# Optimization experiments

Hardware: AMD Instinct MI355X
Metric: run time of the kernel (lower is better)

## Reference

```python
import jax, jax.numpy as jnp
import numpy as np

B, S, D, DS, NSLOT = 2, 1024, 1024, 320, 512
H, CH = 4, 5
DFF = 4 * D
MAXIT = 2


def _ln(x, g, b, eps=1e-5):
    m = x.mean(-1, keepdims=True)
    v = ((x - m) ** 2).mean(-1, keepdims=True)
    return (x - m) * jax.lax.rsqrt(v + eps) * g + b


def _mha(x, Wq, Wk, Wv, Wo, bq, bk, bv, bo, nh):
    b_, s_, d_ = x.shape
    hd = d_ // nh
    q = (x @ Wq + bq).reshape(b_, s_, nh, hd)
    k = (x @ Wk + bk).reshape(b_, s_, nh, hd)
    v = (x @ Wv + bv).reshape(b_, s_, nh, hd)
    a = jax.nn.softmax(jnp.einsum('bqhd,bkhd->bhqk', q, k) * (hd ** -0.5), axis=-1)
    o = jnp.einsum('bhqk,bkhd->bqhd', a, v).reshape(b_, s_, d_)
    return o @ Wo + bo


def setup_inputs():
    key = jax.random.key(0)
    ks = iter(jax.random.split(key, 64))
    n = lambda shape: jax.random.normal(next(ks), shape, jnp.float32) * 0.02
    z = lambda shape: jnp.zeros(shape, jnp.float32)
    o = lambda shape: jnp.ones(shape, jnp.float32)
    return dict(
        x=jax.random.normal(next(ks), (B, S, D), jnp.float32),
        cache=jax.random.normal(next(ks), (B, NSLOT, DS), jnp.float32),
        iter_emb=n((16, D)),
        rq_w=n((D, D)), rg_w=n((D, 1)), rg_b=z((1,)), ck_w=n((DS, D)), cv_w=n((DS, D)),
        aq_w=n((D, D)), ak_w=n((D, D)), av_w=n((D, D)), ao_w=n((D, D)),
        aq_b=z((D,)), ak_b=z((D,)), av_b=z((D,)), ao_b=z((D,)),
        f1_w=n((D, DFF)), f1_b=z((DFF,)), f2_w=n((DFF, D)), f2_b=z((D,)),
        n1_g=o((D,)), n1_b=z((D,)), n2_g=o((D,)), n2_b=z((D,)),
        sq_w=n((DS, DS)), tk_w=n((D, DS)), tv_w=n((D, DS)), wg_w=n((D, 1)), wg_b=z((1,)),
        cq_w=n((DS, DS)), ck2_w=n((DS, DS)), cv2_w=n((DS, DS)), co_w=n((DS, DS)),
        cq_b=z((DS,)), ck2_b=z((DS,)), cv2_b=z((DS,)), co_b=z((DS,)),
        cn_g=o((DS,)), cn_b=z((DS,)),
        max_iterations=MAXIT,
    )


def reference(x, cache, iter_emb, rq_w, rg_w, rg_b, ck_w, cv_w,
              aq_w, ak_w, av_w, ao_w, aq_b, ak_b, av_b, ao_b,
              f1_w, f1_b, f2_w, f2_b, n1_g, n1_b, n2_g, n2_b,
              sq_w, tk_w, tv_w, wg_w, wg_b,
              cq_w, ck2_w, cv2_w, co_w, cq_b, ck2_b, cv2_b, co_b, cn_g, cn_b,
              max_iterations):
    def mem_read(h, cc):
        # gather from cache: gated cross-attention readout
        q = h @ rq_w                                   # [B,S,D]
        k = cc @ ck_w                                  # [B,N,D]
        v = cc @ cv_w                                  # [B,N,D]
        a = jax.nn.softmax(jnp.einsum('bsd,bnd->bsn', q, k) * (D ** -0.5), axis=-1)
        readout = jnp.einsum('bsn,bnd->bsd', a, v)
        gate = jax.nn.sigmoid(h @ rg_w + rg_b)          # [B,S,1] soft read gate
        return h + gate * readout

    def compute_block(h):
        # faithful to ComputeBlock (non-linear-attention branch): norm1 used twice
        hn = _ln(h, n1_g, n1_b)
        attn = _mha(hn, aq_w, ak_w, av_w, ao_w, aq_b, ak_b, av_b, ao_b, H)
        h = _ln(h + attn, n1_g, n1_b)
        ffn = jax.nn.gelu(h @ f1_w + f1_b) @ f2_w + f2_b
        return _ln(h + ffn, n2_g, n2_b)

    def mem_write(h, cc):
        # importance-scored scatter: slots attend over tokens, gated by importance
        sq = cc @ sq_w                                  # [B,N,DS]
        tk = h @ tk_w                                   # [B,S,DS]
        tv = h @ tv_w                                   # [B,S,DS]
        gate = jax.nn.sigmoid(h @ wg_w + wg_b)          # [B,S,1] soft write gate
        a = jax.nn.softmax(jnp.einsum('bnd,bsd->bns', sq, tk) * (DS ** -0.5), axis=-1)
        upd = jnp.einsum('bns,bsd->bnd', a, gate * tv)
        return cc + upd

    def cache_self_attn(cc):
        attn = _mha(cc, cq_w, ck2_w, cv2_w, co_w, cq_b, ck2_b, cv2_b, co_b, CH)
        return _ln(cc + attn, cn_g, cn_b)

    h = x
    cc = cache
    layer_input = x
    h_prev = None
    for it in range(max_iterations):
        h = h + iter_emb[it][None, None, :]
        if it > 0:
            h = h + layer_input + h_prev
        h_enh = mem_read(h, cc)
        h_comp = compute_block(h_enh)
        cc = mem_write(h_comp, cc)
        cc = cache_self_attn(cc)
        h = h_comp
        h_prev = jax.lax.stop_gradient(h_comp)  # torch: h_prev = h_computed.detach()
    return h
```

## Files before the change

### kernel.cpp

```cpp
#include <hip/hip_runtime.h>
#include <cstdint>

constexpr int B_ = 2, S_ = 1024, D_ = 1024, DS_ = 320, NSLOT_ = 512;
constexpr int H_ = 4, CH_ = 5, DFF_ = 4096;
constexpr int HD_ = D_ / H_;
constexpr int CHD_ = DS_ / CH_;
constexpr int BS_ = B_ * S_;
constexpr int BNS_ = B_ * NSLOT_;

typedef unsigned short u16;
typedef __attribute__((ext_vector_type(8))) short bf16x8;
typedef __attribute__((ext_vector_type(4))) float f32x4;
typedef __attribute__((ext_vector_type(4))) u16 u16x4;
typedef long long ll;

__device__ __forceinline__ u16 f2bf(float f) {
  unsigned u = __float_as_uint(f);
  return (u16)((u + 0x7FFFu + ((u >> 16) & 1u)) >> 16);
}
__device__ __forceinline__ float bf2f(u16 h) { return __uint_as_float((unsigned)h << 16); }

__device__ __forceinline__ void gload16(const void* g, void* l) {
  __builtin_amdgcn_global_load_lds((const __attribute__((address_space(1))) void*)g,
                                   (__attribute__((address_space(3))) void*)l, 16, 0, 0);
}

template<int BN>
__global__ __launch_bounds__(512, 4)
void k_gemm(const u16* __restrict__ A, int lda, ll sA, ll sA2,
            const u16* __restrict__ Bp, int ldb, ll sB, ll sB2,
            float* __restrict__ outF, u16* __restrict__ outB,
            int ldc, ll sC, ll sC2,
            u16* __restrict__ outBT, int ldt, ll sT, ll sT2,
            int K, int zdiv, const float* __restrict__ bias,
            const float* __restrict__ rowscale, int rscfrom,
            int splitcol, int act)
{
  constexpr int BM = 128;
  constexpr int MI = (BN == 128) ? 2 : 1;
  constexpr int NI = 4;
  constexpr int WROWS = MI * 16;
  constexpr int ABYT = BM * 128;
  constexpr int BBYT = BN * 128;
  constexpr int BUF = ABYT + BBYT;
  const int z = blockIdx.z, zb = z / zdiv, zr = z - zb * zdiv;
  A  += (ll)zb * sA + (ll)zr * sA2;
  Bp += (ll)zb * sB + (ll)zr * sB2;
  const ll cof = (ll)zb * sC + (ll)zr * sC2;
  const ll tof = (ll)zb * sT + (ll)zr * sT2;
  const int bm = blockIdx.y * BM, bn = blockIdx.x * BN;
  __shared__ __align__(16) char lds[2 * BUF];
  const int tid = threadIdx.x;
  const int lane = tid & 63, wid = tid >> 6;
  const int wm = (BN == 128) ? (wid >> 1) : wid;
  const int wn = (BN == 128) ? (wid & 1) : 0;
  const int rowb = wm * WROWS, colb = wn * 64;

  f32x4 acc[MI][NI];
  const f32x4 fz = {0.f, 0.f, 0.f, 0.f};
  #pragma unroll
  for (int i = 0; i < MI; ++i)
    #pragma unroll
    for (int j = 0; j < NI; ++j) acc[i][j] = fz;

  const int trow = tid >> 3;
  const int tg   = ((tid & 7) ^ (trow & 7)) * 8;
  const u16* gA  = A + (ll)(bm + trow) * lda + tg;
  const u16* gA2 = gA + (ll)64 * lda;
  const u16* gB  = Bp + (ll)(bn + trow) * ldb + tg;
  const u16* gB2 = gB + (ll)64 * ldb;

  const int r = lane & 15, q = lane >> 4;
  const int c7 = r & 7;
  const int gs0 = ((q) ^ c7) << 4;
  const int gs1 = ((4 + q) ^ c7) << 4;
  int aoff[MI], boff[NI];
  #pragma unroll
  for (int i = 0; i < MI; ++i) aoff[i] = (rowb + i * 16 + r) * 128;
  #pragma unroll
  for (int j = 0; j < NI; ++j) boff[j] = (colb + j * 16 + r) * 128;

  auto stage = [&](int buf, int it) {
    char* la = lds + buf * BUF + wid * 1024;
    char* lb = la + ABYT;
    const int ko = it << 6;
    gload16(gA + ko, la);
    gload16(gA2 + ko, la + 8192);
    gload16(gB + ko, lb);
    if constexpr (BN == 128) gload16(gB2 + ko, lb + 8192);
  };

  const int nsteps = K >> 6;
  stage(0, 0);
  int bufp = 0;
  for (int it = 0; it < nsteps; ++it) {
    asm volatile("s_waitcnt vmcnt(0)" ::: "memory");
    __builtin_amdgcn_s_barrier();
    __builtin_amdgcn_sched_barrier(0);
    if (it + 1 < nsteps) stage(bufp ^ 1, it + 1);
    const char* pa = lds + bufp * BUF;
    const char* pb = pa + ABYT;
    #pragma unroll
    for (int s = 0; s < 2; ++s) {
      const int gso = s ? gs1 : gs0;
      bf16x8 af[MI], bv[NI];
      #pragma unroll
      for (int i = 0; i < MI; ++i) af[i] = *(const bf16x8*)(pa + aoff[i] + gso);
      #pragma unroll
      for (int j = 0; j < NI; ++j) bv[j] = *(const bf16x8*)(pb + boff[j] + gso);
      #pragma unroll
      for (int i = 0; i < MI; ++i)
        #pragma unroll
        for (int j = 0; j < NI; ++j)
          acc[i][j] = __builtin_amdgcn_mfma_f32_16x16x32_bf16(af[i], bv[j], acc[i][j], 0, 0, 0);
    }
    asm volatile("s_waitcnt lgkmcnt(0)" ::: "memory");
    __builtin_amdgcn_sched_barrier(0);
    bufp ^= 1;
  }

  const int fr = lane & 15, fq = lane >> 4;
  #pragma unroll
  for (int i = 0; i < MI; ++i) {
    const int r0 = bm + rowb + i * 16 + fq * 4;
    #pragma unroll
    for (int j = 0; j < NI; ++j) {
      const int cn = bn + colb + j * 16 + fr;
      const float bvv = bias ? bias[cn] : 0.f;
      const bool doRs = rowscale && (cn >= rscfrom);
      float vv[4];
      #pragma unroll
      for (int t = 0; t < 4; ++t) {
        float v = acc[i][j][t] + bvv;
        if (doRs) v *= rowscale[r0 + t];
        if (act) v = 0.5f * v * (1.f + tanhf(0.7978845608028654f * (v + 0.044715f * v * v * v)));
        vv[t] = v;
      }
      if (cn < splitcol) {
        if (outF) {
          #pragma unroll
          for (int t = 0; t < 4; ++t) outF[cof + (ll)(r0 + t) * ldc + cn] = vv[t];
        }
        if (outB) {
          #pragma unroll
          for (int t = 0; t < 4; ++t) outB[cof + (ll)(r0 + t) * ldc + cn] = f2bf(vv[t]);
        }
      } else {
        u16x4 pk = {f2bf(vv[0]), f2bf(vv[1]), f2bf(vv[2]), f2bf(vv[3])};
        *(u16x4*)(outBT + tof + (ll)(cn - splitcol) * ldt + r0) = pk;
      }
    }
  }
}

struct PrepTable {
  const float* src[16];
  u16* dst[16];
  int R[16];
  int C[16];
  int off[17];
};

__global__ __launch_bounds__(256)
void k_prep_all(PrepTable T)
{
  __shared__ float t[32][33];
  const int b = blockIdx.x;
  int w = 0;
  #pragma unroll
  for (int i = 1; i < 16; ++i) if (b >= T.off[i]) w = i;
  const int lb = b - T.off[w];
  const int tilesC = T.C[w] >> 5;
  const int by = (lb / tilesC) << 5;
  const int bx = (lb - (lb / tilesC) * tilesC) << 5;
  const float* in = T.src[w];
  u16* out = T.dst[w];
  const int R = T.R[w], C = T.C[w];
  const int tx = threadIdx.x & 31, ty = threadIdx.x >> 5;
  #pragma unroll
  for (int i = 0; i < 32; i += 8)
    t[ty + i][tx] = in[(ll)(by + ty + i) * C + bx + tx];
  __syncthreads();
  #pragma unroll
  for (int i = 0; i < 32; i += 8)
    out[(ll)(bx + ty + i) * R + by + tx] = f2bf(t[tx][ty + i]);
}

__global__ __launch_bounds__(256)
void k_cvt(const float* __restrict__ in, u16* __restrict__ out, int n)
{
  int i = blockIdx.x * 256 + threadIdx.x;
  if (i < n) out[i] = f2bf(in[i]);
}

__global__ __launch_bounds__(256)
void k_cat3f(float* __restrict__ dst, const float* __restrict__ a, int na,
             const float* __restrict__ b, int nb, const float* __restrict__ c, int nc)
{
  int i = blockIdx.x * 256 + threadIdx.x;
  if (i < na) dst[i] = a[i];
  else if (i < na + nb) dst[i] = b[i - na];
  else if (i < na + nb + nc) dst[i] = c[i - na - nb];
}

__global__ __launch_bounds__(256)
void k_softmax_b16(u16* __restrict__ x, int cols, float scale)
{
  u16* p = x + (ll)blockIdx.x * cols;
  const int tid = threadIdx.x;
  __shared__ float red[256];
  float v[4];
  float m = -1e30f;
  #pragma unroll
  for (int i = 0; i < 4; ++i) {
    const int c = tid + (i << 8);
    v[i] = (c < cols) ? bf2f(p[c]) * scale : -1e30f;
    m = fmaxf(m, v[i]);
  }
  red[tid] = m; __syncthreads();
  for (int s = 128; s > 0; s >>= 1) { if (tid < s) red[tid] = fmaxf(red[tid], red[tid + s]); __syncthreads(); }
  m = red[0]; __syncthreads();
  float sum = 0.f;
  #pragma unroll
  for (int i = 0; i < 4; ++i) { v[i] = expf(v[i] - m); sum += v[i]; }
  red[tid] = sum; __syncthreads();
  for (int s = 128; s > 0; s >>= 1) { if (tid < s) red[tid] += red[tid + s]; __syncthreads(); }
  const float inv = 1.f / red[0];
  #pragma unroll
  for (int i = 0; i < 4; ++i) {
    const int c = tid + (i << 8);
    if (c < cols) p[c] = f2bf(v[i] * inv);
  }
}

__global__ __launch_bounds__(256)
void k_layernorm(const float* __restrict__ x, const float* __restrict__ res,
                 const float* __restrict__ res2, const float* __restrict__ rbias,
                 const float* __restrict__ g, const float* __restrict__ b,
                 float* __restrict__ outF, u16* __restrict__ outB, int cols)
{
  const ll ro = (ll)blockIdx.x * cols;
  const float* px = x + ro;
  const float* pr = res ? res + ro : nullptr;
  const float* p2 = res2 ? res2 + ro : nullptr;
  __shared__ float red[256];
  const int tid = threadIdx.x;
  auto val = [&](int c) {
    float v = px[c];
    if (pr) v += pr[c];
    if (p2) v += p2[c];
    if (rbias) v += rbias[c];
    return v;
  };
  float s = 0.f;
  for (int c = tid; c < cols; c += 256) s += val(c);
  red[tid] = s; __syncthreads();
  for (int t = 128; t > 0; t >>= 1) { if (tid < t) red[tid] += red[tid + t]; __syncthreads(); }
  const float mean = red[0] / cols; __syncthreads();
  float s2 = 0.f;
  for (int c = tid; c < cols; c += 256) { float v = val(c) - mean; s2 += v * v; }
  red[tid] = s2; __syncthreads();
  for (int t = 128; t > 0; t >>= 1) { if (tid < t) red[tid] += red[tid + t]; __syncthreads(); }
  const float inv = rsqrtf(red[0] / cols + 1e-5f);
  for (int c = tid; c < cols; c += 256) {
    float v = (val(c) - mean) * inv * g[c] + b[c];
    if (outF) outF[ro + c] = v;
    if (outB) outB[ro + c] = f2bf(v);
  }
}

__global__ __launch_bounds__(256)
void k_gate_add(float* __restrict__ out, const float* __restrict__ h,
                const float* __restrict__ r, const float* __restrict__ w,
                const float* __restrict__ b0, int cols)
{
  const ll ro = (ll)blockIdx.x * cols;
  const float* ph = h + ro;
  const float* pr = r + ro;
  __shared__ float red[256];
  const int tid = threadIdx.x;
  float s = 0.f;
  for (int c = tid; c < cols; c += 256) s += ph[c] * w[c];
  red[tid] = s; __syncthreads();
  for (int t = 128; t > 0; t >>= 1) { if (tid < t) red[tid] += red[tid + t]; __syncthreads(); }
  const float g = 1.0f / (1.0f + expf(-(red[0] + b0[0])));
  for (int c = tid; c < cols; c += 256) out[ro + c] = ph[c] + g * pr[c];
}

__global__ __launch_bounds__(256)
void k_gate(const float* __restrict__ x, const float* __restrict__ w,
            const float* __restrict__ b0, float* __restrict__ out, int cols)
{
  const int lane = threadIdx.x & 63;
  const int wv = threadIdx.x >> 6;
  const ll row = (ll)blockIdx.x * 4 + wv;
  const float* p = x + row * cols;
  float s = 0.f;
  for (int c = lane; c < cols; c += 64) s += p[c] * w[c];
  #pragma unroll
  for (int off = 32; off > 0; off >>= 1) s += __shfl_down(s, off);
  if (lane == 0) out[row] = 1.0f / (1.0f + expf(-(s + b0[0])));
}

__global__ __launch_bounds__(256)
void k_combine2(float* __restrict__ oF, u16* __restrict__ oB,
                const float* __restrict__ a, float sa, const float* __restrict__ b,
                const float* __restrict__ emb, int n, int Dm1)
{
  int i = blockIdx.x * 256 + threadIdx.x;
  if (i >= n) return;
  float v = sa * a[i];
  if (b) v += b[i];
  v += emb[i & Dm1];
  oF[i] = v; oB[i] = f2bf(v);
}

__global__ __launch_bounds__(256)
void k_add2(float* __restrict__ oF, u16* __restrict__ oB,
            const float* __restrict__ a, const float* __restrict__ b, int n)
{
  int i = blockIdx.x * 256 + threadIdx.x;
  if (i >= n) return;
  float v = a[i] + b[i];
  oF[i] = v; oB[i] = f2bf(v);
}

extern "C" void kernel_launch(void* const* d_in, const int* in_sizes, int n_in,
                              void* d_out, int out_size, void* d_ws, size_t ws_size,
                              hipStream_t stream)
{
  (void)in_sizes; (void)n_in; (void)out_size;
  const float* x        = (const float*)d_in[0];
  const float* cache0   = (const float*)d_in[1];
  const float* iter_emb = (const float*)d_in[2];
  const float* rq_w     = (const float*)d_in[3];
  const float* rg_w     = (const float*)d_in[4];
  const float* rg_b     = (const float*)d_in[5];
  const float* ck_w     = (const float*)d_in[6];
  const float* cv_w     = (const float*)d_in[7];
  const float* aq_w     = (const float*)d_in[8];
  const float* ak_w     = (const float*)d_in[9];
  const float* av_w     = (const float*)d_in[10];
  const float* ao_w     = (const float*)d_in[11];
  const float* aq_b     = (const float*)d_in[12];
  const float* ak_b     = (const float*)d_in[13];
  const float* av_b     = (const float*)d_in[14];
  const float* ao_b     = (const float*)d_in[15];
  const float* f1_w     = (const float*)d_in[16];
  const float* f1_b     = (const float*)d_in[17];
  const float* f2_w     = (const float*)d_in[18];
  const float* f2_b     = (const float*)d_in[19];
  const float* n1_g     = (const float*)d_in[20];
  const float* n1_b     = (const float*)d_in[21];
  const float* n2_g     = (const float*)d_in[22];
  const float* n2_b     = (const float*)d_in[23];
  const float* sq_w     = (const float*)d_in[24];
  const float* tk_w     = (const float*)d_in[25];
  const float* tv_w     = (const float*)d_in[26];
  const float* wg_w     = (const float*)d_in[27];
  const float* wg_b     = (const float*)d_in[28];
  const float* cq_w     = (const float*)d_in[29];
  const float* ck2_w    = (const float*)d_in[30];
  const float* cv2_w    = (const float*)d_in[31];
  const float* co_w     = (const float*)d_in[32];
  const float* cq_b     = (const float*)d_in[33];
  const float* ck2_b    = (const float*)d_in[34];
  const float* cv2_b    = (const float*)d_in[35];
  const float* co_b     = (const float*)d_in[36];
  const float* cn_g     = (const float*)d_in[37];
  const float* cn_b     = (const float*)d_in[38];

  float* out = (float*)d_out;

  size_t off = 0;
  char* base = (char*)d_ws;
  auto allocF = [&](size_t n) { float* p = (float*)(base + off); off += n * 4; off = (off + 255) & ~(size_t)255; return p; };
  auto allocH = [&](size_t n) { u16* p = (u16*)(base + off); off += n * 2; off = (off + 255) & ~(size_t)255; return p; };

  float* hbuf  = allocF((size_t)BS_ * D_);
  float* henh  = allocF((size_t)BS_ * D_);
  float* hcomp = allocF((size_t)BS_ * D_);
  float* h2b   = allocF((size_t)BS_ * D_);
  float* tA    = allocF((size_t)2 * BS_ * D_);
  float* gate  = allocF((size_t)BS_);
  float* ccnf  = allocF((size_t)BNS_ * DS_);
  float* updf  = allocF((size_t)BNS_ * DS_);
  float* coo   = allocF((size_t)BNS_ * DS_);
  float* ccwf  = allocF((size_t)BNS_ * DS_);
  float* qkvb  = allocF(3 * D_);
  float* cqkvb = allocF(3 * DS_);
  u16* rqT  = allocH((size_t)D_ * D_);
  u16* ckT  = allocH((size_t)D_ * DS_);
  u16* cvT  = allocH((size_t)D_ * DS_);
  u16* aqT  = allocH((size_t)D_ * D_);
  u16* akT  = allocH((size_t)D_ * D_);
  u16* avT  = allocH((size_t)D_ * D_);
  u16* aoT  = allocH((size_t)D_ * D_);
  u16* f1T  = allocH((size_t)DFF_ * D_);
  u16* f2T  = allocH((size_t)D_ * DFF_);
  u16* sqT  = allocH((size_t)DS_ * DS_);
  u16* tkT  = allocH((size_t)DS_ * D_);
  u16* tvTw = allocH((size_t)DS_ * D_);
  u16* cqT  = allocH((size_t)DS_ * DS_);
  u16* ck2T = allocH((size_t)DS_ * DS_);
  u16* cv2T = allocH((size_t)DS_ * DS_);
  u16* coT  = allocH((size_t)DS_ * DS_);
  u16* bb1  = allocH((size_t)BS_ * D_);
  u16* bb2  = allocH((size_t)BS_ * D_);
  u16* bb3  = allocH((size_t)BS_ * D_);
  u16* bb4  = allocH((size_t)BS_ * D_);
  u16* bb5  = allocH((size_t)B_ * H_ * S_ * S_);
  u16* bbQK = allocH((size_t)BS_ * 2 * D_);
  u16* bbCQK= allocH((size_t)BNS_ * 2 * DS_);
  u16* cc0b = allocH((size_t)BNS_ * DS_);
  u16* ccwb = allocH((size_t)BNS_ * DS_);
  u16* sqb  = allocH((size_t)BNS_ * DS_);
  u16* tkb  = allocH((size_t)BS_ * DS_);
  u16* tvTb = allocH((size_t)DS_ * BS_);
  u16* ccnb = allocH((size_t)BNS_ * DS_);
  u16* cv2Tb= allocH((size_t)DS_ * BNS_);
  u16* csab = allocH((size_t)BNS_ * DS_);
  if (off > ws_size) return;
  (void)cvT; (void)akT; (void)avT; (void)tvTw; (void)ck2T; (void)cv2T;

  auto gemm = [&](int M, int N, int K, int z, int zdiv,
                  const u16* Ap, int lda, ll sa, ll sa2,
                  const u16* Bq, int ldb, ll sb, ll sb2,
                  float* oF, u16* oB, int ldc, ll sc, ll sc2,
                  u16* oBT, int ldt, ll st, ll st2,
                  const float* bias, const float* rsc, int rscfrom,
                  int splitcol, int act) {
    const ll b64 = (ll)(N / 64) * (M / 128) * z;
    if (N % 128 == 0 && b64 > 768 && (splitcol % 128) == 0) {
      dim3 g(N / 128, M / 128, z);
      k_gemm<128><<<g, 512, 0, stream>>>(Ap, lda, sa, sa2, Bq, ldb, sb, sb2,
          oF, oB, ldc, sc, sc2, oBT, ldt, st, st2, K, zdiv, bias, rsc, rscfrom, splitcol, act);
    } else {
      dim3 g(N / 64, M / 128, z);
      k_gemm<64><<<g, 512, 0, stream>>>(Ap, lda, sa, sa2, Bq, ldb, sb, sb2,
          oF, oB, ldc, sc, sc2, oBT, ldt, st, st2, K, zdiv, bias, rsc, rscfrom, splitcol, act);
    }
  };
  auto lnorm = [&](const float* xp, const float* rp, const float* rp2, const float* rb,
                   const float* g, const float* b, float* oF, u16* oB, int rows, int cols) {
    k_layernorm<<<rows, 256, 0, stream>>>(xp, rp, rp2, rb, g, b, oF, oB, cols);
  };
  auto eg = [](int n) { return dim3((n + 255) / 256); };

  {
    PrepTable T;
    const float* srcs[16] = {rq_w, ck_w, cv_w, aq_w, ak_w, av_w, ao_w, f1_w,
                             f2_w, sq_w, tk_w, tv_w, cq_w, ck2_w, cv2_w, co_w};
    u16* dsts[16] = {rqT, ckT, cvT, aqT, akT, avT, aoT, f1T,
                     f2T, sqT, tkT, tvTw, cqT, ck2T, cv2T, coT};
    const int Rs[16] = {D_, DS_, DS_, D_, D_, D_, D_, D_, DFF_, DS_, D_, D_, DS_, DS_, DS_, DS_};
    const int Cs[16] = {D_, D_, D_, D_, D_, D_, D_, DFF_, D_, DS_, DS_, DS_, DS_, DS_, DS_, DS_};
    int acc0 = 0;
    for (int i = 0; i < 16; ++i) {
      T.src[i] = srcs[i]; T.dst[i] = dsts[i]; T.R[i] = Rs[i]; T.C[i] = Cs[i];
      T.off[i] = acc0;
      acc0 += (Rs[i] >> 5) * (Cs[i] >> 5);
    }
    T.off[16] = acc0;
    k_prep_all<<<acc0, 256, 0, stream>>>(T);
  }
  k_cvt<<<eg(BNS_ * DS_), 256, 0, stream>>>(cache0, cc0b, BNS_ * DS_);
  k_cat3f<<<eg(3 * D_), 256, 0, stream>>>(qkvb, aq_b, D_, ak_b, D_, av_b, D_);
  k_cat3f<<<eg(3 * DS_), 256, 0, stream>>>(cqkvb, cq_b, DS_, ck2_b, DS_, cv2_b, DS_);

  auto mem_read = [&](const float* h_f, const u16* h_b, const u16* cc_b, float* o_henh) {
    gemm(BS_, D_, D_, 1, 1, h_b, D_, 0, 0, rqT, D_, 0, 0,
         nullptr, bb2, D_, 0, 0, nullptr, 0, 0, 0,
         nullptr, nullptr, 0, D_, 0);
    gemm(BNS_, 2 * D_, DS_, 1, 1, cc_b, DS_, 0, 0, ckT, DS_, 0, 0,
         nullptr, bb3, D_, 0, 0, bb4, BNS_, 0, 0,
         nullptr, nullptr, 0, D_, 0);
    gemm(S_, NSLOT_, D_, B_, 1, bb2, D_, (ll)S_ * D_, 0,
         bb3, D_, (ll)NSLOT_ * D_, 0,
         nullptr, bb5, NSLOT_, (ll)S_ * NSLOT_, 0, nullptr, 0, 0, 0,
         nullptr, nullptr, 0, NSLOT_, 0);
    k_softmax_b16<<<B_ * S_, 256, 0, stream>>>(bb5, NSLOT_, 0.03125f);
    gemm(S_, D_, NSLOT_, B_, 1, bb5, NSLOT_, (ll)S_ * NSLOT_, 0,
         bb4, BNS_, NSLOT_, 0,
         tA, nullptr, D_, (ll)S_ * D_, 0, nullptr, 0, 0, 0,
         nullptr, nullptr, 0, D_, 0);
    k_gate_add<<<BS_, 256, 0, stream>>>(o_henh, h_f, tA, rg_w, rg_b, D_);
  };

  auto compute_block = [&](const float* he, float* oF, u16* oB) {
    lnorm(he, nullptr, nullptr, nullptr, n1_g, n1_b, nullptr, bb1, BS_, D_);
    gemm(BS_, 3 * D_, D_, 1, 1, bb1, D_, 0, 0, aqT, D_, 0, 0,
         nullptr, bbQK, 2 * D_, 0, 0, bb4, BS_, 0, 0,
         qkvb, nullptr, 0, 2 * D_, 0);
    gemm(S_, S_, HD_, B_ * H_, H_,
         bbQK, 2 * D_, (ll)S_ * 2 * D_, HD_,
         bbQK + D_, 2 * D_, (ll)S_ * 2 * D_, HD_,
         nullptr, bb5, S_, (ll)H_ * S_ * S_, (ll)S_ * S_, nullptr, 0, 0, 0,
         nullptr, nullptr, 0, S_, 0);
    k_softmax_b16<<<B_ * H_ * S_, 256, 0, stream>>>(bb5, S_, 0.0625f);
    gemm(S_, HD_, S_, B_ * H_, H_,
         bb5, S_, (ll)H_ * S_ * S_, (ll)S_ * S_,
         bb4, BS_, S_, (ll)HD_ * BS_,
         nullptr, bb2, D_, (ll)S_ * D_, HD_, nullptr, 0, 0, 0,
         nullptr, nullptr, 0, HD_, 0);
    gemm(BS_, D_, D_, 1, 1, bb2, D_, 0, 0, aoT, D_, 0, 0,
         tA, nullptr, D_, 0, 0, nullptr, 0, 0, 0,
         ao_b, nullptr, 0, D_, 0);
    lnorm(he, tA, nullptr, nullptr, n1_g, n1_b, h2b, bb1, BS_, D_);
    gemm(BS_, DFF_, D_, 1, 1, bb1, D_, 0, 0, f1T, D_, 0, 0,
         nullptr, bb5, DFF_, 0, 0, nullptr, 0, 0, 0,
         f1_b, nullptr, 0, DFF_, 1);
    gemm(BS_, D_, 2048, 2, 2, bb5, DFF_, 0, 2048, f2T, DFF_, 0, 2048,
         tA, nullptr, D_, 0, (ll)BS_ * D_, nullptr, 0, 0, 0,
         nullptr, nullptr, 0, D_, 0);
    lnorm(h2b, tA, tA + (ll)BS_ * D_, f2_b, n2_g, n2_b, oF, oB, BS_, D_);
  };

  auto mem_write_csa = [&](const float* hc_f, const u16* hc_b,
                           const float* ccin_f, const u16* ccin_b) {
    gemm(BNS_, DS_, DS_, 1, 1, ccin_b, DS_, 0, 0, sqT, DS_, 0, 0,
         nullptr, sqb, DS_, 0, 0, nullptr, 0, 0, 0,
         nullptr, nullptr, 0, DS_, 0);
    k_gate<<<BS_ / 4, 256, 0, stream>>>(hc_f, wg_w, wg_b, gate, D_);
    gemm(BS_, 2 * DS_, D_, 1, 1, hc_b, D_, 0, 0, tkT, D_, 0, 0,
         nullptr, tkb, DS_, 0, 0, tvTb, BS_, 0, 0,
         nullptr, gate, DS_, DS_, 0);
    gemm(NSLOT_, S_, DS_, B_, 1, sqb, DS_, (ll)NSLOT_ * DS_, 0,
         tkb, DS_, (ll)S_ * DS_, 0,
         nullptr, bb5, S_, (ll)NSLOT_ * S_, 0, nullptr, 0, 0, 0,
         nullptr, nullptr, 0, S_, 0);
    k_softmax_b16<<<B_ * NSLOT_, 256, 0, stream>>>(bb5, S_, 0.05590169943749474f);
    gemm(NSLOT_, DS_, S_, B_, 1, bb5, S_, (ll)NSLOT_ * S_, 0,
         tvTb, BS_, S_, 0,
         updf, nullptr, DS_, (ll)NSLOT_ * DS_, 0, nullptr, 0, 0, 0,
         nullptr, nullptr, 0, DS_, 0);
    k_add2<<<eg(BNS_ * DS_), 256, 0, stream>>>(ccnf, ccnb, ccin_f, updf, BNS_ * DS_);
    gemm(BNS_, 3 * DS_, DS_, 1, 1, ccnb, DS_, 0, 0, cqT, DS_, 0, 0,
         nullptr, bbCQK, 2 * DS_, 0, 0, cv2Tb, BNS_, 0, 0,
         cqkvb, nullptr, 0, 2 * DS_, 0);
    gemm(NSLOT_, NSLOT_, CHD_, B_ * CH_, CH_,
         bbCQK, 2 * DS_, (ll)NSLOT_ * 2 * DS_, CHD_,
         bbCQK + DS_, 2 * DS_, (ll)NSLOT_ * 2 * DS_, CHD_,
         nullptr, bb5, NSLOT_, (ll)CH_ * NSLOT_ * NSLOT_, (ll)NSLOT_ * NSLOT_,
         nullptr, 0, 0, 0, nullptr, nullptr, 0, NSLOT_, 0);
    k_softmax_b16<<<B_ * CH_ * NSLOT_, 256, 0, stream>>>(bb5, NSLOT_, 0.125f);
    gemm(NSLOT_, CHD_, NSLOT_, B_ * CH_, CH_,
         bb5, NSLOT_, (ll)CH_ * NSLOT_ * NSLOT_, (ll)NSLOT_ * NSLOT_,
         cv2Tb, BNS_, NSLOT_, (ll)CHD_ * BNS_,
         nullptr, csab, DS_, (ll)NSLOT_ * DS_, CHD_, nullptr, 0, 0, 0,
         nullptr, nullptr, 0, CHD_, 0);
    gemm(BNS_, DS_, DS_, 1, 1, csab, DS_, 0, 0, coT, DS_, 0, 0,
         coo, nullptr, DS_, 0, 0, nullptr, 0, 0, 0,
         co_b, nullptr, 0, DS_, 0);
    lnorm(ccnf, coo, nullptr, nullptr, cn_g, cn_b, ccwf, ccwb, BNS_, DS_);
  };

  k_combine2<<<eg(BS_ * D_), 256, 0, stream>>>(hbuf, bb1, x, 1.0f, nullptr, iter_emb, BS_ * D_, D_ - 1);
  mem_read(hbuf, bb1, cc0b, henh);
  compute_block(henh, hcomp, bb3);
  mem_write_csa(hcomp, bb3, cache0, cc0b);

  k_combine2<<<eg(BS_ * D_), 256, 0, stream>>>(hbuf, bb1, hcomp, 2.0f, x, iter_emb + D_, BS_ * D_, D_ - 1);
  mem_read(hbuf, bb1, ccwb, henh);
  compute_block(henh, out, nullptr);
}
```

Baseline: 553.0 us.

## Add 256x128-tile triple-buffered GEMM for QKV, attention scores and FFN1

Adds a new GEMM kernel with a 256x128 output tile, 8 waves each owning 64x64, and a three-stage LDS ring filled by global_load_lds. Loads are split into two half-steps that overlap with the MFMA work, and setprio is raised around the MFMA bursts. The QKV projection, the QK^T score GEMM and the FFN first layer now use it. Larger tiles raise arithmetic intensity per LDS byte, but use about 144KB of LDS and give fewer blocks, which lowers occupancy and can cause wave-quantization tail effects on the smaller GEMMs.

```diff
diff --git a/kernel.cpp b/kernel.cpp
--- a/kernel.cpp
+++ b/kernel.cpp
@@ -23,6 +23,157 @@
 __device__ __forceinline__ void gload16(const void* g, void* l) {
   __builtin_amdgcn_global_load_lds((const __attribute__((address_space(1))) void*)g,
                                    (__attribute__((address_space(3))) void*)l, 16, 0, 0);
+}
+
+__global__ __launch_bounds__(512, 2)
+void k_gemm8(const u16* __restrict__ A, int lda, ll sA, ll sA2,
+             const u16* __restrict__ Bp, int ldb, ll sB, ll sB2,
+             float* __restrict__ outF, u16* __restrict__ outB,
+             int ldc, ll sC, ll sC2,
+             u16* __restrict__ outBT, int ldt, ll sT, ll sT2,
+             int K, int zdiv, const float* __restrict__ bias,
+             int splitcol, int act)
+{
+  constexpr int ABYT = 256 * 128;
+  constexpr int BBYT = 128 * 128;
+  constexpr int BUF = ABYT + BBYT;
+  const int z = blockIdx.z, zb = z / zdiv, zr = z - zb * zdiv;
+  A  += (ll)zb * sA + (ll)zr * sA2;
+  Bp += (ll)zb * sB + (ll)zr * sB2;
+  const ll cof = (ll)zb * sC + (ll)zr * sC2;
+  const ll tof = (ll)zb * sT + (ll)zr * sT2;
+  const int bm = blockIdx.y * 256, bn = blockIdx.x * 128;
+  __shared__ __align__(16) char lds[3 * BUF];
+  const int tid = threadIdx.x, lane = tid & 63, wid = tid >> 6;
+  const int wm = wid >> 1, wn = wid & 1;
+
+  f32x4 acc[4][4];
+  const f32x4 fz = {0.f, 0.f, 0.f, 0.f};
+  #pragma unroll
+  for (int i = 0; i < 4; ++i)
+    #pragma unroll
+    for (int j = 0; j < 4; ++j) acc[i][j] = fz;
+
+  const int trow = tid >> 3;
+  const int tg   = ((tid & 7) ^ (trow & 7)) * 8;
+  const u16* gA0 = A + (ll)(bm + trow) * lda + tg;
+  const u16* gA1 = gA0 + (ll)64 * lda;
+  const u16* gA2p = gA0 + (ll)128 * lda;
+  const u16* gA3 = gA0 + (ll)192 * lda;
+  const u16* gB0 = Bp + (ll)(bn + trow) * ldb + tg;
+  const u16* gB1 = gB0 + (ll)64 * ldb;
+
+  const int r = lane & 15, q = lane >> 4, c7 = r & 7;
+  const int gs0 = (q ^ c7) << 4;
+  const int gs1 = ((4 + q) ^ c7) << 4;
+  int aoff[4], boff[4];
+  #pragma unroll
+  for (int i = 0; i < 4; ++i) aoff[i] = (wm * 64 + i * 16 + r) * 128;
+  #pragma unroll
+  for (int j = 0; j < 4; ++j) boff[j] = ABYT + (wn * 64 + j * 16 + r) * 128;
+
+  auto s3a = [&](int buf, int t) {
+    char* d = lds + buf * BUF + wid * 1024;
+    const int ko = t << 6;
+    gload16(gA0 + ko, d);
+    gload16(gA1 + ko, d + 8192);
+    gload16(gA2p + ko, d + 16384);
+  };
+  auto s3b = [&](int buf, int t) {
+    char* d = lds + buf * BUF + wid * 1024;
+    const int ko = t << 6;
+    gload16(gA3 + ko, d + 24576);
+    gload16(gB0 + ko, d + ABYT);
+    gload16(gB1 + ko, d + ABYT + 8192);
+  };
+
+  const int nst = K >> 6;
+  s3a(0, 0); s3b(0, 0);
+  if (nst > 1) {
+    s3a(1, 1); s3b(1, 1);
+    asm volatile("s_waitcnt vmcnt(6)" ::: "memory");
+  } else {
+    asm volatile("s_waitcnt vmcnt(0)" ::: "memory");
+  }
+  __builtin_amdgcn_s_barrier();
+
+  for (int t = 0; t < nst; ++t) {
+    int p = t; while (p >= 3) p -= 3;
+    int nb = p + 2; if (nb >= 3) nb -= 3;
+    const bool st = (t + 2) < nst;
+    const char* pa = lds + p * BUF;
+    {
+      bf16x8 av[4], bv[4];
+      #pragma unroll
+      for (int i = 0; i < 4; ++i) av[i] = *(const bf16x8*)(pa + aoff[i] + gs0);
+      #pragma unroll
+      for (int j = 0; j < 4; ++j) bv[j] = *(const bf16x8*)(pa + boff[j] + gs0);
+      if (st) s3a(nb, t + 2);
+      __builtin_amdgcn_s_barrier();
+      asm volatile("s_waitcnt lgkmcnt(0)" ::: "memory");
+      __builtin_amdgcn_sched_barrier(0);
+      __builtin_amdgcn_s_setprio(1);
+      #pragma unroll
+      for (int i = 0; i < 4; ++i)
+        #pragma unroll
+        for (int j = 0; j < 4; ++j)
+          acc[i][j] = __builtin_amdgcn_mfma_f32_16x16x32_bf16(av[i], bv[j], acc[i][j], 0, 0, 0);
+      __builtin_amdgcn_s_setprio(0);
+      __builtin_amdgcn_s_barrier();
+    }
+    {
+      bf16x8 av[4], bv[4];
+      #pragma unroll
+      for (int i = 0; i < 4; ++i) av[i] = *(const bf16x8*)(pa + aoff[i] + gs1);
+      #pragma unroll
+      for (int j = 0; j < 4; ++j) bv[j] = *(const bf16x8*)(pa + boff[j] + gs1);
+      if (st) s3b(nb, t + 2);
+      if (st) asm volatile("s_waitcnt vmcnt(6)" ::: "memory");
+      else    asm volatile("s_waitcnt vmcnt(0)" ::: "memory");
+      __builtin_amdgcn_s_barrier();
+      asm volatile("s_waitcnt lgkmcnt(0)" ::: "memory");
+      __builtin_amdgcn_sched_barrier(0);
+      __builtin_amdgcn_s_setprio(1);
+      #pragma unroll
+      for (int i = 0; i < 4; ++i)
+        #pragma unroll
+        for (int j = 0; j < 4; ++j)
+          acc[i][j] = __builtin_amdgcn_mfma_f32_16x16x32_bf16(av[i], bv[j], acc[i][j], 0, 0, 0);
+      __builtin_amdgcn_s_setprio(0);
+      __builtin_amdgcn_s_barrier();
+    }
+  }
+
+  const int fr = lane & 15, fq = lane >> 4;
+  #pragma unroll
+  for (int i = 0; i < 4; ++i) {
+    const int r0 = bm + wm * 64 + i * 16 + fq * 4;
+    #pragma unroll
+    for (int j = 0; j < 4; ++j) {
+      const int cn = bn + wn * 64 + j * 16 + fr;
+      const float bvv = bias ? bias[cn] : 0.f;
+      float vv[4];
+      #pragma unroll
+      for (int t = 0; t < 4; ++t) {
+        float v = acc[i][j][t] + bvv;
+        if (act) v = 0.5f * v * (1.f + tanhf(0.7978845608028654f * (v + 0.044715f * v * v * v)));
+        vv[t] = v;
+      }
+      if (cn < splitcol) {
+        if (outF) {
+          #pragma unroll
+          for (int t = 0; t < 4; ++t) outF[cof + (ll)(r0 + t) * ldc + cn] = vv[t];
+        }
+        if (outB) {
+          #pragma unroll
+          for (int t = 0; t < 4; ++t) outB[cof + (ll)(r0 + t) * ldc + cn] = f2bf(vv[t]);
+        }
+      } else {
+        u16x4 pk = {f2bf(vv[0]), f2bf(vv[1]), f2bf(vv[2]), f2bf(vv[3])};
+        *(u16x4*)(outBT + tof + (ll)(cn - splitcol) * ldt + r0) = pk;
+      }
+    }
+  }
 }
 
 template<int BN>
@@ -441,6 +592,16 @@
           oF, oB, ldc, sc, sc2, oBT, ldt, st, st2, K, zdiv, bias, rsc, rscfrom, splitcol, act);
     }
   };
+  auto gemm8 = [&](int M, int N, int K, int z, int zdiv,
+                   const u16* Ap, int lda, ll sa, ll sa2,
+                   const u16* Bq, int ldb, ll sb, ll sb2,
+                   float* oF, u16* oB, int ldc, ll sc, ll sc2,
+                   u16* oBT, int ldt, ll st, ll st2,
+                   const float* bias, int splitcol, int act) {
+    dim3 g(N / 128, M / 256, z);
+    k_gemm8<<<g, 512, 0, stream>>>(Ap, lda, sa, sa2, Bq, ldb, sb, sb2,
+        oF, oB, ldc, sc, sc2, oBT, ldt, st, st2, K, zdiv, bias, splitcol, act);
+  };
   auto lnorm = [&](const float* xp, const float* rp, const float* rp2, const float* rb,
                    const float* g, const float* b, float* oF, u16* oB, int rows, int cols) {
     k_layernorm<<<rows, 256, 0, stream>>>(xp, rp, rp2, rb, g, b, oF, oB, cols);
@@ -489,14 +650,14 @@
 
   auto compute_block = [&](const float* he, float* oF, u16* oB) {
     lnorm(he, nullptr, nullptr, nullptr, n1_g, n1_b, nullptr, bb1, BS_, D_);
-    gemm(BS_, 3 * D_, D_, 1, 1, bb1, D_, 0, 0, aqT, D_, 0, 0,
-         nullptr, bbQK, 2 * D_, 0, 0, bb4, BS_, 0, 0,
-         qkvb, nullptr, 0, 2 * D_, 0);
-    gemm(S_, S_, HD_, B_ * H_, H_,
-         bbQK, 2 * D_, (ll)S_ * 2 * D_, HD_,
-         bbQK + D_, 2 * D_, (ll)S_ * 2 * D_, HD_,
-         nullptr, bb5, S_, (ll)H_ * S_ * S_, (ll)S_ * S_, nullptr, 0, 0, 0,
-         nullptr, nullptr, 0, S_, 0);
+    gemm8(BS_, 3 * D_, D_, 1, 1, bb1, D_, 0, 0, aqT, D_, 0, 0,
+          nullptr, bbQK, 2 * D_, 0, 0, bb4, BS_, 0, 0,
+          qkvb, 2 * D_, 0);
+    gemm8(S_, S_, HD_, B_ * H_, H_,
+          bbQK, 2 * D_, (ll)S_ * 2 * D_, HD_,
+          bbQK + D_, 2 * D_, (ll)S_ * 2 * D_, HD_,
+          nullptr, bb5, S_, (ll)H_ * S_ * S_, (ll)S_ * S_,
+          nullptr, 0, 0, 0, nullptr, S_, 0);
     k_softmax_b16<<<B_ * H_ * S_, 256, 0, stream>>>(bb5, S_, 0.0625f);
     gemm(S_, HD_, S_, B_ * H_, H_,
          bb5, S_, (ll)H_ * S_ * S_, (ll)S_ * S_,
@@ -507,9 +668,9 @@
          tA, nullptr, D_, 0, 0, nullptr, 0, 0, 0,
          ao_b, nullptr, 0, D_, 0);
     lnorm(he, tA, nullptr, nullptr, n1_g, n1_b, h2b, bb1, BS_, D_);
-    gemm(BS_, DFF_, D_, 1, 1, bb1, D_, 0, 0, f1T, D_, 0, 0,
-         nullptr, bb5, DFF_, 0, 0, nullptr, 0, 0, 0,
-         f1_b, nullptr, 0, DFF_, 1);
+    gemm8(BS_, DFF_, D_, 1, 1, bb1, D_, 0, 0, f1T, D_, 0, 0,
+          nullptr, bb5, DFF_, 0, 0, nullptr, 0, 0, 0,
+          f1_b, DFF_, 1);
     gemm(BS_, D_, 2048, 2, 2, bb5, DFF_, 0, 2048, f2T, DFF_, 0, 2048,
          tA, nullptr, D_, 0, (ll)BS_ * D_, nullptr, 0, 0, 0,
          nullptr, nullptr, 0, D_, 0);
```

Result: slower. 573.2 us (+3.7%).

## Triple-buffer GEMM K-loop and drop the 128-wide tile variant

Applied to the files above, without the earlier changes.

The GEMM kernel moves from double to triple buffering in LDS. Loads run two K-steps ahead, and each step waits with a partial vmcnt instead of draining all outstanding loads. The 128x128 tile variant is removed, so every GEMM uses 128x64 tiles. This is meant to hide global-load latency better, but large GEMMs lose the higher per-block data reuse of the wider tile and use more LDS per block, which can reduce occupancy.

```diff
diff --git a/kernel.cpp b/kernel.cpp
--- a/kernel.cpp
+++ b/kernel.cpp
@@ -25,7 +25,6 @@
                                    (__attribute__((address_space(3))) void*)l, 16, 0, 0);
 }
 
-template<int BN>
 __global__ __launch_bounds__(512, 4)
 void k_gemm(const u16* __restrict__ A, int lda, ll sA, ll sA2,
             const u16* __restrict__ Bp, int ldb, ll sB, ll sB2,
@@ -36,49 +35,39 @@
             const float* __restrict__ rowscale, int rscfrom,
             int splitcol, int act)
 {
-  constexpr int BM = 128;
-  constexpr int MI = (BN == 128) ? 2 : 1;
-  constexpr int NI = 4;
-  constexpr int WROWS = MI * 16;
-  constexpr int ABYT = BM * 128;
-  constexpr int BBYT = BN * 128;
+  constexpr int ABYT = 128 * 128;
+  constexpr int BBYT = 64 * 128;
   constexpr int BUF = ABYT + BBYT;
   const int z = blockIdx.z, zb = z / zdiv, zr = z - zb * zdiv;
   A  += (ll)zb * sA + (ll)zr * sA2;
   Bp += (ll)zb * sB + (ll)zr * sB2;
   const ll cof = (ll)zb * sC + (ll)zr * sC2;
   const ll tof = (ll)zb * sT + (ll)zr * sT2;
-  const int bm = blockIdx.y * BM, bn = blockIdx.x * BN;
-  __shared__ __align__(16) char lds[2 * BUF];
+  const int bm = blockIdx.y * 128, bn = blockIdx.x * 64;
+  __shared__ __align__(16) char lds[3 * BUF];
   const int tid = threadIdx.x;
   const int lane = tid & 63, wid = tid >> 6;
-  const int wm = (BN == 128) ? (wid >> 1) : wid;
-  const int wn = (BN == 128) ? (wid & 1) : 0;
-  const int rowb = wm * WROWS, colb = wn * 64;
-
-  f32x4 acc[MI][NI];
+  const int rowb = wid * 16;
+
+  f32x4 acc[4];
   const f32x4 fz = {0.f, 0.f, 0.f, 0.f};
   #pragma unroll
-  for (int i = 0; i < MI; ++i)
-    #pragma unroll
-    for (int j = 0; j < NI; ++j) acc[i][j] = fz;
+  for (int j = 0; j < 4; ++j) acc[j] = fz;
 
   const int trow = tid >> 3;
   const int tg   = ((tid & 7) ^ (trow & 7)) * 8;
   const u16* gA  = A + (ll)(bm + trow) * lda + tg;
   const u16* gA2 = gA + (ll)64 * lda;
   const u16* gB  = Bp + (ll)(bn + trow) * ldb + tg;
-  const u16* gB2 = gB + (ll)64 * ldb;
 
   const int r = lane & 15, q = lane >> 4;
   const int c7 = r & 7;
   const int gs0 = ((q) ^ c7) << 4;
   const int gs1 = ((4 + q) ^ c7) << 4;
-  int aoff[MI], boff[NI];
-  #pragma unroll
-  for (int i = 0; i < MI; ++i) aoff[i] = (rowb + i * 16 + r) * 128;
-  #pragma unroll
-  for (int j = 0; j < NI; ++j) boff[j] = (colb + j * 16 + r) * 128;
+  const int aoff = (rowb + r) * 128;
+  int boff[4];
+  #pragma unroll
+  for (int j = 0; j < 4; ++j) boff[j] = ABYT + (j * 16 + r) * 128;
 
   auto stage = [&](int buf, int it) {
     char* la = lds + buf * BUF + wid * 1024;
@@ -87,68 +76,64 @@
     gload16(gA + ko, la);
     gload16(gA2 + ko, la + 8192);
     gload16(gB + ko, lb);
-    if constexpr (BN == 128) gload16(gB2 + ko, lb + 8192);
   };
 
   const int nsteps = K >> 6;
   stage(0, 0);
-  int bufp = 0;
+  if (nsteps > 1) stage(1, 1);
   for (int it = 0; it < nsteps; ++it) {
-    asm volatile("s_waitcnt vmcnt(0)" ::: "memory");
+    if (it == nsteps - 1) asm volatile("s_waitcnt vmcnt(0)" ::: "memory");
+    else                  asm volatile("s_waitcnt vmcnt(3)" ::: "memory");
     __builtin_amdgcn_s_barrier();
     __builtin_amdgcn_sched_barrier(0);
-    if (it + 1 < nsteps) stage(bufp ^ 1, it + 1);
-    const char* pa = lds + bufp * BUF;
-    const char* pb = pa + ABYT;
+    if (it + 2 < nsteps) {
+      int nb = it + 2; while (nb >= 3) nb -= 3;
+      stage(nb, it + 2);
+    }
+    int p = it; while (p >= 3) p -= 3;
+    const char* pa = lds + p * BUF;
     #pragma unroll
     for (int s = 0; s < 2; ++s) {
       const int gso = s ? gs1 : gs0;
-      bf16x8 af[MI], bv[NI];
+      bf16x8 af = *(const bf16x8*)(pa + aoff + gso);
+      bf16x8 bv[4];
       #pragma unroll
-      for (int i = 0; i < MI; ++i) af[i] = *(const bf16x8*)(pa + aoff[i] + gso);
+      for (int j = 0; j < 4; ++j) bv[j] = *(const bf16x8*)(pa + boff[j] + gso);
       #pragma unroll
-      for (int j = 0; j < NI; ++j) bv[j] = *(const bf16x8*)(pb + boff[j] + gso);
-      #pragma unroll
-      for (int i = 0; i < MI; ++i)
-        #pragma unroll
-        for (int j = 0; j < NI; ++j)
-          acc[i][j] = __builtin_amdgcn_mfma_f32_16x16x32_bf16(af[i], bv[j], acc[i][j], 0, 0, 0);
+      for (int j = 0; j < 4; ++j)
+        acc[j] = __builtin_amdgcn_mfma_f32_16x16x32_bf16(af, bv[j], acc[j], 0, 0, 0);
     }
     asm volatile("s_waitcnt lgkmcnt(0)" ::: "memory");
     __builtin_amdgcn_sched_barrier(0);
-    bufp ^= 1;
   }
 
   const int fr = lane & 15, fq = lane >> 4;
-  #pragma unroll
-  for (int i = 0; i < MI; ++i) {
-    const int r0 = bm + rowb + i * 16 + fq * 4;
+  const int r0 = bm + rowb + fq * 4;
+  #pragma unroll
+  for (int j = 0; j < 4; ++j) {
+    const int cn = bn + j * 16 + fr;
+    const float bvv = bias ? bias[cn] : 0.f;
+    const bool doRs = rowscale && (cn >= rscfrom);
+    float vv[4];
     #pragma unroll
-    for (int j = 0; j < NI; ++j) {
-      const int cn = bn + colb + j * 16 + fr;
-      const float bvv = bias ? bias[cn] : 0.f;
-      const bool doRs = rowscale && (cn >= rscfrom);
-      float vv[4];
-      #pragma unroll
-      for (int t = 0; t < 4; ++t) {
-        float v = acc[i][j][t] + bvv;
-        if (doRs) v *= rowscale[r0 + t];
-        if (act) v = 0.5f * v * (1.f + tanhf(0.7978845608028654f * (v + 0.044715f * v * v * v)));
-        vv[t] = v;
+    for (int t = 0; t < 4; ++t) {
+      float v = acc[j][t] + bvv;
+      if (doRs) v *= rowscale[r0 + t];
+      if (act) v = 0.5f * v * (1.f + tanhf(0.7978845608028654f * (v + 0.044715f * v * v * v)));
+      vv[t] = v;
+    }
+    if (cn < splitcol) {
+      if (outF) {
+        #pragma unroll
+        for (int t = 0; t < 4; ++t) outF[cof + (ll)(r0 + t) * ldc + cn] = vv[t];
       }
-      if (cn < splitcol) {
-        if (outF) {
-          #pragma unroll
-          for (int t = 0; t < 4; ++t) outF[cof + (ll)(r0 + t) * ldc + cn] = vv[t];
-        }
-        if (outB) {
-          #pragma unroll
-          for (int t = 0; t < 4; ++t) outB[cof + (ll)(r0 + t) * ldc + cn] = f2bf(vv[t]);
-        }
-      } else {
-        u16x4 pk = {f2bf(vv[0]), f2bf(vv[1]), f2bf(vv[2]), f2bf(vv[3])};
-        *(u16x4*)(outBT + tof + (ll)(cn - splitcol) * ldt + r0) = pk;
+      if (outB) {
+        #pragma unroll
+        for (int t = 0; t < 4; ++t) outB[cof + (ll)(r0 + t) * ldc + cn] = f2bf(vv[t]);
       }
+    } else {
+      u16x4 pk = {f2bf(vv[0]), f2bf(vv[1]), f2bf(vv[2]), f2bf(vv[3])};
+      *(u16x4*)(outBT + tof + (ll)(cn - splitcol) * ldt + r0) = pk;
     }
   }
 }
@@ -430,16 +415,9 @@
                   u16* oBT, int ldt, ll st, ll st2,
                   const float* bias, const float* rsc, int rscfrom,
                   int splitcol, int act) {
-    const ll b64 = (ll)(N / 64) * (M / 128) * z;
-    if (N % 128 == 0 && b64 > 768 && (splitcol % 128) == 0) {
-      dim3 g(N / 128, M / 128, z);
-      k_gemm<128><<<g, 512, 0, stream>>>(Ap, lda, sa, sa2, Bq, ldb, sb, sb2,
-          oF, oB, ldc, sc, sc2, oBT, ldt, st, st2, K, zdiv, bias, rsc, rscfrom, splitcol, act);
-    } else {
-      dim3 g(N / 64, M / 128, z);
-      k_gemm<64><<<g, 512, 0, stream>>>(Ap, lda, sa, sa2, Bq, ldb, sb, sb2,
-          oF, oB, ldc, sc, sc2, oBT, ldt, st, st2, K, zdiv, bias, rsc, rscfrom, splitcol, act);
-    }
+    dim3 g(N / 64, M / 128, z);
+    k_gemm<<<g, 512, 0, stream>>>(Ap, lda, sa, sa2, Bq, ldb, sb, sb2,
+        oF, oB, ldc, sc, sc2, oBT, ldt, st, st2, K, zdiv, bias, rsc, rscfrom, splitcol, act);
   };
   auto lnorm = [&](const float* xp, const float* rp, const float* rp2, const float* rb,
                    const float* g, const float* b, float* oF, u16* oB, int rows, int cols) {
```

After: 542.6 us. No clear change (-1.9%).
